# Performance work log

Measured on AMD Instinct MI355X. Metric: run time of the kernel, lower is better.

## Reference

```python
import jax, jax.numpy as jnp
import numpy as np

B, N, D = 16, 200000, 18  # batch, n_water, ndims (9 pos + 9 vel)


def setup_inputs() -> dict:
    key = jax.random.key(0)
    k1, _ = jax.random.split(key)
    x = jax.random.normal(k1, (B, N, D), dtype=jnp.float32)
    # rigid water geometry: two O-H bond lengths and the H-H distance
    l = jnp.asarray([0.9572, 0.9572, 1.5139], dtype=jnp.float32)
    return {"x": x, "l": l}


def reference(x, l):
    # _extract_positions: position_idx = (0..8), contiguous slice then reshape
    b, n, _ = x.shape
    r = x[:, :, :9].reshape(b, n, 3, 3)  # [b, n, particle, xyz]
    # _delta_r: internal pairwise deltas within each water molecule
    dr = jnp.stack(
        (r[:, :, 0] - r[:, :, 1],
         r[:, :, 1] - r[:, :, 2],
         r[:, :, 2] - r[:, :, 0]),
        axis=2,
    )  # [b, n, 3, 3]
    drnorm = jnp.sqrt(jnp.sum(dr * dr, axis=-1))  # [b, n, 3]
    c = drnorm - l  # broadcast l over [b, n, 3]
    return c
```

## Files before the change

### kernel.cpp

```cpp
#include <hip/hip_runtime.h>


constexpr int F_PER_MOL = 18;
constexpr int BLOCK = 256;

__global__ __launch_bounds__(BLOCK) void water_kernel(
    const float* __restrict__ x,
    const float* __restrict__ l,
    float* __restrict__ out,
    long long total_mol)
{
    const long long mol = (long long)blockIdx.x * BLOCK + threadIdx.x;
    if (mol >= total_mol) return;

    const float* __restrict__ m = x + mol * F_PER_MOL;
    const float2 p01 = *reinterpret_cast<const float2*>(m + 0);
    const float2 p23 = *reinterpret_cast<const float2*>(m + 2);
    const float2 p45 = *reinterpret_cast<const float2*>(m + 4);
    const float2 p67 = *reinterpret_cast<const float2*>(m + 6);
    const float  p8  = m[8];

    const float ox = p01.x, oy = p01.y, oz = p23.x;
    const float ax = p23.y, ay = p45.x, az = p45.y;
    const float bx = p67.x, by = p67.y, bz = p8;

    const float d0x = ox - ax, d0y = oy - ay, d0z = oz - az;
    const float d1x = ax - bx, d1y = ay - by, d1z = az - bz;
    const float d2x = bx - ox, d2y = by - oy, d2z = bz - oz;

    const float n0 = sqrtf(d0x * d0x + d0y * d0y + d0z * d0z);
    const float n1 = sqrtf(d1x * d1x + d1y * d1y + d1z * d1z);
    const float n2 = sqrtf(d2x * d2x + d2y * d2y + d2z * d2z);

    const float l0 = l[0], l1 = l[1], l2 = l[2];

    float* o = out + mol * 3;
    o[0] = n0 - l0;
    o[1] = n1 - l1;
    o[2] = n2 - l2;
}

extern "C" void kernel_launch(void* const* d_in, const int* in_sizes, int n_in,
                              void* d_out, int out_size, void* d_ws, size_t ws_size,
                              hipStream_t stream)
{
    const float* x = (const float*)d_in[0];
    const float* l = (const float*)d_in[1];
    float* out = (float*)d_out;

    const long long total_mol = (long long)in_sizes[0] / F_PER_MOL;
    const int grid = (int)((total_mol + BLOCK - 1) / BLOCK);

    water_kernel<<<grid, BLOCK, 0, stream>>>(x, l, out, total_mol);
}
```

Baseline: 317.4 us.

## Stage molecule tiles through shared memory for coalesced float4 loads and stores

Each block now loads a 512-molecule tile of the input with contiguous float4 reads into LDS, computes the three constraint residuals from LDS, and writes outputs back through LDS as coalesced float4 stores. This replaces strided per-thread float2 loads and scalar 3-float stores that made poorly coalesced memory transactions. It also reads the unused velocity fields and uses about 42KB of LDS per block, which may limit occupancy.

Result: no change. 322.6 us (+1.6%).

```diff
diff --git a/kernel.cpp b/kernel.cpp
--- a/kernel.cpp
+++ b/kernel.cpp
@@ -2,7 +2,11 @@
 
 
 constexpr int F_PER_MOL = 18;
-constexpr int BLOCK = 256;
+constexpr int BLOCK     = 256;
+constexpr int TILE      = 512;
+constexpr int IN_F4     = TILE * F_PER_MOL / 4;
+constexpr int OUT_F     = TILE * 3;
+constexpr int OUT_F4    = OUT_F / 4;
 
 __global__ __launch_bounds__(BLOCK) void water_kernel(
     const float* __restrict__ x,
@@ -10,34 +14,79 @@
     float* __restrict__ out,
     long long total_mol)
 {
-    const long long mol = (long long)blockIdx.x * BLOCK + threadIdx.x;
-    if (mol >= total_mol) return;
+    __shared__ float4 sx[IN_F4];
+    __shared__ float  so[OUT_F];
 
-    const float* __restrict__ m = x + mol * F_PER_MOL;
-    const float2 p01 = *reinterpret_cast<const float2*>(m + 0);
-    const float2 p23 = *reinterpret_cast<const float2*>(m + 2);
-    const float2 p45 = *reinterpret_cast<const float2*>(m + 4);
-    const float2 p67 = *reinterpret_cast<const float2*>(m + 6);
-    const float  p8  = m[8];
+    const int t = threadIdx.x;
+    const long long tile_base   = (long long)blockIdx.x * TILE;
+    const long long total_in_f  = total_mol * F_PER_MOL;
+    const long long total_out_f = total_mol * 3;
 
-    const float ox = p01.x, oy = p01.y, oz = p23.x;
-    const float ax = p23.y, ay = p45.x, az = p45.y;
-    const float bx = p67.x, by = p67.y, bz = p8;
+    const long long in_f4_base = (tile_base * F_PER_MOL) >> 2;
+    const float4* __restrict__ x4 = reinterpret_cast<const float4*>(x);
 
-    const float d0x = ox - ax, d0y = oy - ay, d0z = oz - az;
-    const float d1x = ax - bx, d1y = ay - by, d1z = az - bz;
-    const float d2x = bx - ox, d2y = by - oy, d2z = bz - oz;
-
-    const float n0 = sqrtf(d0x * d0x + d0y * d0y + d0z * d0z);
-    const float n1 = sqrtf(d1x * d1x + d1y * d1y + d1z * d1z);
-    const float n2 = sqrtf(d2x * d2x + d2y * d2y + d2z * d2z);
+#pragma unroll
+    for (int i = 0; i < IN_F4 / BLOCK; ++i) {
+        const int s = i * BLOCK + t;
+        const long long g  = in_f4_base + s;
+        const long long gf = g * 4;
+        if (gf + 4 <= total_in_f) {
+            sx[s] = x4[g];
+        } else {
+            float4 v = make_float4(0.f, 0.f, 0.f, 0.f);
+            if (gf + 0 < total_in_f) v.x = x[gf + 0];
+            if (gf + 1 < total_in_f) v.y = x[gf + 1];
+            if (gf + 2 < total_in_f) v.z = x[gf + 2];
+            if (gf + 3 < total_in_f) v.w = x[gf + 3];
+            sx[s] = v;
+        }
+    }
+    __syncthreads();
 
     const float l0 = l[0], l1 = l[1], l2 = l[2];
+    const float* sxf = reinterpret_cast<const float*>(sx);
 
-    float* o = out + mol * 3;
-    o[0] = n0 - l0;
-    o[1] = n1 - l1;
-    o[2] = n2 - l2;
+#pragma unroll
+    for (int h = 0; h < TILE / BLOCK; ++h) {
+        const int j = t + h * BLOCK;
+        const float* m = sxf + j * F_PER_MOL;
+
+        const float ox = m[0], oy = m[1], oz = m[2];
+        const float ax = m[3], ay = m[4], az = m[5];
+        const float bx = m[6], by = m[7], bz = m[8];
+
+        const float d0x = ox - ax, d0y = oy - ay, d0z = oz - az;
+        const float d1x = ax - bx, d1y = ay - by, d1z = az - bz;
+        const float d2x = bx - ox, d2y = by - oy, d2z = bz - oz;
+
+        const float n0 = sqrtf(d0x * d0x + d0y * d0y + d0z * d0z);
+        const float n1 = sqrtf(d1x * d1x + d1y * d1y + d1z * d1z);
+        const float n2 = sqrtf(d2x * d2x + d2y * d2y + d2z * d2z);
+
+        so[j * 3 + 0] = n0 - l0;
+        so[j * 3 + 1] = n1 - l1;
+        so[j * 3 + 2] = n2 - l2;
+    }
+    __syncthreads();
+
+    const long long out_f4_base = (tile_base * 3) >> 2;
+    float4* __restrict__ out4 = reinterpret_cast<float4*>(out);
+    const float4* so4 = reinterpret_cast<const float4*>(so);
+
+#pragma unroll
+    for (int i = 0; i < OUT_F4; i += BLOCK) {
+        const int s = i + t;
+        if (s >= OUT_F4) continue;
+        const long long g  = out_f4_base + s;
+        const long long gf = g * 4;
+        if (gf + 4 <= total_out_f) {
+            out4[g] = so4[s];
+        } else if (gf < total_out_f) {
+            const float* sof = reinterpret_cast<const float*>(so);
+            const int rem = (int)(total_out_f - gf);
+            for (int k = 0; k < rem; ++k) out[gf + k] = sof[s * 4 + k];
+        }
+    }
 }
 
 extern "C" void kernel_launch(void* const* d_in, const int* in_sizes, int n_in,
@@ -49,7 +98,7 @@
     float* out = (float*)d_out;
 
     const long long total_mol = (long long)in_sizes[0] / F_PER_MOL;
-    const int grid = (int)((total_mol + BLOCK - 1) / BLOCK);
+    const int grid = (int)((total_mol + TILE - 1) / TILE);
 
     water_kernel<<<grid, BLOCK, 0, stream>>>(x, l, out, total_mol);
 }
```
